# Optimization experiments

Measured on AMD Instinct MI355X. Metric: run time of the kernel, lower is better.

## Reference

```python
import jax, jax.numpy as jnp
import numpy as np

EMBED_DICT = 200
EMBED_DIM = 16
HIDDEN = 32
LSTM_DIM = 256
B, C, L = 8192, 16, 64
END_IDX = 1  # stand-in for token_list.index('<End>')


def _lin(k, i, o):
    return jax.random.normal(k, (i, o), jnp.float32) * (1.0 / np.sqrt(i))


def setup_inputs() -> dict:
    key = jax.random.key(0)
    ks = jax.random.split(key, 20)
    feat_in = EMBED_DIM * 14 + LSTM_DIM  # 480
    z = lambda n: jnp.zeros((n,), jnp.float32)
    return {
        "trees": jax.random.randint(ks[0], (B, 1 + C, 17), 0, L),
        "lstm_out_list": jax.random.normal(ks[1], (B, L, 1, LSTM_DIM), jnp.float32),
        "first_notes": jax.random.normal(ks[2], (B, EMBED_DIM), jnp.float32),
        "train": 1,
        "embedding": jax.random.normal(ks[3], (EMBED_DICT, EMBED_DIM), jnp.float32) * 0.05,
        "leaf_end_W": _lin(ks[4], EMBED_DIM, HIDDEN), "leaf_end_b": z(HIDDEN),
        "lc_W1": _lin(ks[5], feat_in, HIDDEN * 4), "lc_b1": z(HIDDEN * 4),
        "lc_W2": _lin(ks[6], HIDDEN * 4, HIDDEN), "lc_b2": z(HIDDEN),
        "cs_W1": _lin(ks[7], HIDDEN * 2, HIDDEN * 4), "cs_b1": z(HIDDEN * 4),
        "cs_W2": _lin(ks[8], HIDDEN * 4, HIDDEN), "cs_b2": z(HIDDEN),
        "nf_W1": _lin(ks[9], feat_in, HIDDEN * 4), "nf_b1": z(HIDDEN * 4),
        "nf_W2": _lin(ks[10], HIDDEN * 4, HIDDEN), "nf_b2": z(HIDDEN),
        "cb_W1": _lin(ks[11], HIDDEN * 2, HIDDEN * 4), "cb_b1": z(HIDDEN * 4),
        "cb_W2": _lin(ks[12], HIDDEN * 4, HIDDEN), "cb_b2": z(HIDDEN),
        "ff_W1": _lin(ks[13], HIDDEN, HIDDEN), "ff_b1": z(HIDDEN),
        "ff_W2": _lin(ks[14], HIDDEN, HIDDEN), "ff_b2": z(HIDDEN),
        "ts_W": _lin(ks[15], HIDDEN, 1), "ts_b": z(1),
    }


def _mlp2(x, W1, b1, W2, b2):
    # Linear -> ReLU -> Linear -> ReLU (matches nn.Sequential blocks)
    return jax.nn.relu(jax.nn.relu(x @ W1 + b1) @ W2 + b2)


def reference(trees, lstm_out_list, first_notes, train, embedding,
              leaf_end_W, leaf_end_b, lc_W1, lc_b1, lc_W2, lc_b2,
              cs_W1, cs_b1, cs_W2, cs_b2, nf_W1, nf_b1, nf_W2, nf_b2,
              cb_W1, cb_b1, cb_W2, cb_b2, ff_W1, ff_b1, ff_W2, ff_b2,
              ts_W, ts_b):
    Bn = trees.shape[0]
    root = trees[:, 0, :]        # (B, 17)
    leaves = trees[:, 1:, :]     # (B, C, 17)
    Cn = leaves.shape[1]
    bidx = jnp.arange(Bn)

    # ---- leaf nodes: either leaf_end_ff(embed(type)) or leaf_child_ff(concat) ----
    leaf_tok = embedding[leaves[:, :, 2:-1]].reshape(Bn, Cn, -1)       # (B,C,224)
    leaf_ptr = lstm_out_list[bidx[:, None], leaves[:, :, -1], 0, :]    # (B,C,256)
    leaf_child = _mlp2(jnp.concatenate([leaf_tok, leaf_ptr], -1),
                       lc_W1, lc_b1, lc_W2, lc_b2)                     # (B,C,32)
    leaf_end = embedding[leaves[:, :, 2]] @ leaf_end_W + leaf_end_b    # (B,C,32)
    is_end = (leaves[:, :, 2] == END_IDX)[..., None]
    children = jnp.where(is_end, leaf_end, leaf_child)                 # (B,C,32)

    # ---- sequential left fold with child_sum_ff over children ----
    def step(carry, child):
        nxt = _mlp2(jnp.concatenate([carry, child], -1), cs_W1, cs_b1, cs_W2, cs_b2)
        return nxt, None
    child_summary, _ = jax.lax.scan(step, children[:, 0],
                                    jnp.moveaxis(children[:, 1:], 0, 1))  # (B,32)

    # ---- root node embedding + combine ----
    node_tok = embedding[root[:, 2:-1]].reshape(Bn, -1)                # (B,224)
    node_ptr = lstm_out_list[bidx, root[:, -1], 0, :]                  # (B,256)
    node_tmp = _mlp2(jnp.concatenate([node_tok, node_ptr], -1),
                     nf_W1, nf_b1, nf_W2, nf_b2)                       # (B,32)
    tree_sum = _mlp2(jnp.concatenate([node_tmp, child_summary], -1),
                     cb_W1, cb_b1, cb_W2, cb_b2)                       # (B,32)

    # ---- head: two linears (no activation) then score ----
    ff = (tree_sum @ ff_W1 + ff_b1) @ ff_W2 + ff_b2
    return ff @ ts_W + ts_b                                            # (B,1)
```

## Files before the change

kernel.cpp:

```cpp
#include <hip/hip_runtime.h>
#include <cstddef>


typedef __bf16 bf16x8 __attribute__((ext_vector_type(8)));
typedef float  f32x4  __attribute__((ext_vector_type(4)));

__global__ __launch_bounds__(256) void prep_kernel(
    const float* __restrict__ embedding,
    const float* __restrict__ leaf_end_W, const float* __restrict__ leaf_end_b,
    const float* __restrict__ lc_W1, const float* __restrict__ lc_W2,
    const float* __restrict__ nf_W1, const float* __restrict__ nf_W2,
    const float* __restrict__ cs_W1, const float* __restrict__ cs_W2,
    const float* __restrict__ cb_W1, const float* __restrict__ cb_W2,
    const float* __restrict__ ff_W1, const float* __restrict__ ff_b1,
    const float* __restrict__ ff_W2, const float* __restrict__ ff_b2,
    const float* __restrict__ ts_W, const float* __restrict__ ts_b,
    __bf16* __restrict__ lcW1T, __bf16* __restrict__ nfW1T,
    __bf16* __restrict__ lcW2T, __bf16* __restrict__ nfW2T,
    __bf16* __restrict__ emb_bf, float* __restrict__ endvec,
    __bf16* __restrict__ csW1Th, __bf16* __restrict__ csW1Tl,
    __bf16* __restrict__ cbW1Th, __bf16* __restrict__ cbW1Tl,
    __bf16* __restrict__ csW2Th, __bf16* __restrict__ csW2Tl,
    __bf16* __restrict__ cbW2Th, __bf16* __restrict__ cbW2Tl,
    float* __restrict__ vfin, float* __restrict__ cfin)
{
    const int id = blockIdx.x * 256 + threadIdx.x;
    if (id < 61440) {
        const int n = id / 480, k = id - n * 480;
        lcW1T[id] = (__bf16)lc_W1[k * 128 + n];
    } else if (id < 122880) {
        const int e = id - 61440;
        const int n = e / 480, k = e - n * 480;
        nfW1T[e] = (__bf16)nf_W1[k * 128 + n];
    } else if (id < 126976) {
        const int e = id - 122880;
        const int n = e / 128, k = e - n * 128;
        lcW2T[e] = (__bf16)lc_W2[k * 32 + n];
    } else if (id < 131072) {
        const int e = id - 126976;
        const int n = e / 128, k = e - n * 128;
        nfW2T[e] = (__bf16)nf_W2[k * 32 + n];
    } else if (id < 134272) {
        emb_bf[id - 131072] = (__bf16)embedding[id - 131072];
    } else if (id < 134304) {
        const int c = id - 134272;
        float a = leaf_end_b[c];
        #pragma unroll
        for (int d = 0; d < 16; ++d) a = fmaf(embedding[16 + d], leaf_end_W[d * 32 + c], a);
        endvec[c] = a;
    } else if (id < 142496) {
        const int e = id - 134304;
        const int n = e >> 6, k = e & 63;
        const float v = cs_W1[k * 128 + n];
        const __bf16 h = (__bf16)v;
        csW1Th[e] = h; csW1Tl[e] = (__bf16)(v - (float)h);
    } else if (id < 150688) {
        const int e = id - 142496;
        const int n = e >> 6, k = e & 63;
        const float v = cb_W1[k * 128 + n];
        const __bf16 h = (__bf16)v;
        cbW1Th[e] = h; cbW1Tl[e] = (__bf16)(v - (float)h);
    } else if (id < 154784) {
        const int e = id - 150688;
        const int n = e >> 7, k = e & 127;
        const float v = cs_W2[k * 32 + n];
        const __bf16 h = (__bf16)v;
        csW2Th[e] = h; csW2Tl[e] = (__bf16)(v - (float)h);
    } else if (id < 158880) {
        const int e = id - 154784;
        const int n = e >> 7, k = e & 127;
        const float v = cb_W2[k * 32 + n];
        const __bf16 h = (__bf16)v;
        cbW2Th[e] = h; cbW2Tl[e] = (__bf16)(v - (float)h);
    } else if (id < 158912) {
        const int c = id - 158880;
        float w2t[32];
        #pragma unroll
        for (int k = 0; k < 32; ++k) {
            float a = 0.f;
            for (int j = 0; j < 32; ++j) a = fmaf(ff_W2[k * 32 + j], ts_W[j], a);
            w2t[k] = a;
        }
        float a = 0.f;
        #pragma unroll
        for (int k = 0; k < 32; ++k) a = fmaf(ff_W1[c * 32 + k], w2t[k], a);
        vfin[c] = a;
    } else if (id == 158912) {
        float a = ts_b[0];
        for (int j = 0; j < 32; ++j) a = fmaf(ff_b2[j], ts_W[j], a);
        for (int k = 0; k < 32; ++k) {
            float w2t = 0.f;
            for (int j = 0; j < 32; ++j) w2t = fmaf(ff_W2[k * 32 + j], ts_W[j], w2t);
            a = fmaf(ff_b1[k], w2t, a);
        }
        cfin[0] = a;
    }
}

__global__ __launch_bounds__(256) void mlp1_mfma(
    const int* __restrict__ trees,
    const float* __restrict__ lstm,
    const __bf16* __restrict__ lcW1T, const __bf16* __restrict__ nfW1T,
    const __bf16* __restrict__ lcW2T, const __bf16* __restrict__ nfW2T,
    const __bf16* __restrict__ emb_bf, const float* __restrict__ endvec,
    const float* __restrict__ lc_b1, const float* __restrict__ lc_b2,
    const float* __restrict__ nf_b1, const float* __restrict__ nf_b2,
    float* __restrict__ children,
    float* __restrict__ node_tmp)
{
    __shared__ __align__(16) __bf16 emb_s[3200];
    __shared__ __align__(16) __bf16 Hs[64][136];
    __shared__ float b1s[128], b2s[32], evs[32];
    __shared__ int   endf[64];

    const int tid = threadIdx.x;
    const int blk = blockIdx.x;
    const bool leaf = (blk < 2048);

    const __bf16* __restrict__ W1T = leaf ? lcW1T : nfW1T;
    const __bf16* __restrict__ W2T = leaf ? lcW2T : nfW2T;
    const float*  __restrict__ b1p = leaf ? lc_b1 : nf_b1;
    const float*  __restrict__ b2p = leaf ? lc_b2 : nf_b2;

    for (int i = tid; i < 3200; i += 256) emb_s[i] = emb_bf[i];
    if (tid < 128) b1s[tid] = b1p[tid];
    if (tid < 32)  { b2s[tid] = b2p[tid]; evs[tid] = leaf ? endvec[tid] : 0.f; }
    if (tid < 64) {
        if (leaf) {
            const int R = blk * 64 + tid;
            const int b = R >> 4, trow = 1 + (R & 15);
            endf[tid] = (trees[(b * 17 + trow) * 17 + 2] == 1);
        } else endf[tid] = 0;
    }

    const int l  = tid & 63;
    const int w  = tid >> 6;
    const int wm = w >> 1;
    const int wn = w & 1;
    const int lm = l & 15;
    const int kb = l >> 4;

    const int* tb[2];
    const float* lb[2];
    #pragma unroll
    for (int i = 0; i < 2; ++i) {
        const int r = wm * 32 + i * 16 + lm;
        int b, trow;
        if (leaf) { const int R = blk * 64 + r; b = R >> 4; trow = 1 + (R & 15); }
        else      { b = (blk - 2048) * 64 + r; trow = 0; }
        const int* t = trees + (b * 17 + trow) * 17;
        tb[i] = t;
        lb[i] = lstm + ((size_t)b * 64 + (size_t)t[16]) * 256;
    }

    f32x4 acc[2][4];
    #pragma unroll
    for (int i = 0; i < 2; ++i)
        #pragma unroll
        for (int j = 0; j < 4; ++j) acc[i][j] = (f32x4){0.f, 0.f, 0.f, 0.f};

    __syncthreads();

    #pragma unroll
    for (int c = 0; c < 15; ++c) {
        bf16x8 bfr[4];
        #pragma unroll
        for (int ct = 0; ct < 4; ++ct) {
            const int n = wn * 64 + ct * 16 + lm;
            bfr[ct] = *(const bf16x8*)(W1T + n * 480 + c * 32 + kb * 8);
        }
        bf16x8 afr[2];
        if (c < 7) {
            #pragma unroll
            for (int i = 0; i < 2; ++i) {
                const int tok = tb[i][2 + 2 * c + (kb >> 1)];
                afr[i] = *(const bf16x8*)(emb_s + tok * 16 + (kb & 1) * 8);
            }
        } else {
            #pragma unroll
            for (int i = 0; i < 2; ++i) {
                const float* p = lb[i] + (c - 7) * 32 + kb * 8;
                const float4 u = *(const float4*)p;
                const float4 v = *(const float4*)(p + 4);
                bf16x8 t;
                t[0] = (__bf16)u.x; t[1] = (__bf16)u.y; t[2] = (__bf16)u.z; t[3] = (__bf16)u.w;
                t[4] = (__bf16)v.x; t[5] = (__bf16)v.y; t[6] = (__bf16)v.z; t[7] = (__bf16)v.w;
                afr[i] = t;
            }
        }
        #pragma unroll
        for (int i = 0; i < 2; ++i)
            #pragma unroll
            for (int ct = 0; ct < 4; ++ct)
                acc[i][ct] = __builtin_amdgcn_mfma_f32_16x16x32_bf16(afr[i], bfr[ct], acc[i][ct], 0, 0, 0);
    }

    #pragma unroll
    for (int i = 0; i < 2; ++i)
        #pragma unroll
        for (int ct = 0; ct < 4; ++ct) {
            const int col = wn * 64 + ct * 16 + lm;
            const float bias = b1s[col];
            #pragma unroll
            for (int rg = 0; rg < 4; ++rg) {
                float v = acc[i][ct][rg] + bias;
                v = v > 0.f ? v : 0.f;
                Hs[wm * 32 + i * 16 + 4 * kb + rg][col] = (__bf16)v;
            }
        }
    __syncthreads();

    f32x4 acc2[2];
    acc2[0] = (f32x4){0.f, 0.f, 0.f, 0.f};
    acc2[1] = (f32x4){0.f, 0.f, 0.f, 0.f};

    #pragma unroll
    for (int kc = 0; kc < 4; ++kc) {
        const bf16x8 a2 = *(const bf16x8*)(&Hs[w * 16 + lm][kc * 32 + kb * 8]);
        #pragma unroll
        for (int j = 0; j < 2; ++j) {
            const bf16x8 b2 = *(const bf16x8*)(W2T + (j * 16 + lm) * 128 + kc * 32 + kb * 8);
            acc2[j] = __builtin_amdgcn_mfma_f32_16x16x32_bf16(a2, b2, acc2[j], 0, 0, 0);
        }
    }

    #pragma unroll
    for (int j = 0; j < 2; ++j) {
        const int col = j * 16 + lm;
        const float bias = b2s[col];
        #pragma unroll
        for (int rg = 0; rg < 4; ++rg) {
            const int row = w * 16 + 4 * kb + rg;
            float v = acc2[j][rg] + bias;
            v = v > 0.f ? v : 0.f;
            if (leaf) {
                const size_t R = (size_t)blk * 64 + row;
                children[R * 32 + col] = endf[row] ? evs[col] : v;
            } else {
                const size_t R = (size_t)(blk - 2048) * 64 + row;
                node_tmp[R * 32 + col] = v;
            }
        }
    }
}

__global__ __launch_bounds__(512) void scan_mfma(
    const float* __restrict__ children,
    const float* __restrict__ node_tmp,
    const __bf16* __restrict__ csW1Th, const __bf16* __restrict__ csW1Tl,
    const __bf16* __restrict__ csW2Th, const __bf16* __restrict__ csW2Tl,
    const __bf16* __restrict__ cbW1Th, const __bf16* __restrict__ cbW1Tl,
    const __bf16* __restrict__ cbW2Th, const __bf16* __restrict__ cbW2Tl,
    const float* __restrict__ cs_b1, const float* __restrict__ cs_b2,
    const float* __restrict__ cb_b1, const float* __restrict__ cb_b2,
    const float* __restrict__ vfin_g, const float* __restrict__ cfin_g,
    float* __restrict__ out)
{
    __shared__ __align__(16) __bf16 Xh[64][72], Xl[64][72];
    __shared__ __align__(16) __bf16 Hh[64][136], Hl[64][136];
    __shared__ float b1a[128], b1b[128], b2a[32], b2b[32], vfin[32];
    __shared__ float psum[2][64];
    __shared__ float cfin_s;

    const int tid = threadIdx.x;
    const int l = tid & 63, w = tid >> 6;
    const int lm = l & 15, kb = l >> 4;

    if (tid < 128)      { b1a[tid] = cs_b1[tid]; b1b[tid] = cb_b1[tid]; }
    else if (tid < 160) { b2a[tid - 128] = cs_b2[tid - 128]; b2b[tid - 128] = cb_b2[tid - 128]; }
    else if (tid < 192) { vfin[tid - 160] = vfin_g[tid - 160]; }
    else if (tid == 192) cfin_s = cfin_g[0];

    bf16x8 W1r[2][2][2];
    {
        const int q = w & 3;
        #pragma unroll
        for (int nt = 0; nt < 2; ++nt)
            #pragma unroll
            for (int kc = 0; kc < 2; ++kc) {
                const int n = q * 32 + nt * 16 + lm;
                W1r[nt][kc][0] = *(const bf16x8*)(csW1Th + n * 64 + kc * 32 + kb * 8);
                W1r[nt][kc][1] = *(const bf16x8*)(csW1Tl + n * 64 + kc * 32 + kb * 8);
            }
    }
    bf16x8 W2r[4][2];
    {
        const int n2 = (w & 1) * 16 + lm;
        #pragma unroll
        for (int kc = 0; kc < 4; ++kc) {
            W2r[kc][0] = *(const bf16x8*)(csW2Th + n2 * 128 + kc * 32 + kb * 8);
            W2r[kc][1] = *(const bf16x8*)(csW2Tl + n2 * 128 + kc * 32 + kb * 8);
        }
    }

    const size_t base = (size_t)blockIdx.x * 64;
    const int tt = tid >> 3, c4 = (tid & 7) * 4;

    {
        const float4 v0 = *(const float4*)&children[((base + tt) * 16 + 0) * 32 + c4];
        const float4 v1 = *(const float4*)&children[((base + tt) * 16 + 1) * 32 + c4];
        const float a0[4] = {v0.x, v0.y, v0.z, v0.w};
        const float a1[4] = {v1.x, v1.y, v1.z, v1.w};
        union { __bf16 b[4]; short4 s; } h0, l0, h1, l1;
        #pragma unroll
        for (int j = 0; j < 4; ++j) {
            h0.b[j] = (__bf16)a0[j]; l0.b[j] = (__bf16)(a0[j] - (float)h0.b[j]);
            h1.b[j] = (__bf16)a1[j]; l1.b[j] = (__bf16)(a1[j] - (float)h1.b[j]);
        }
        *(short4*)&Xh[tt][c4]      = h0.s;
        *(short4*)&Xl[tt][c4]      = l0.s;
        *(short4*)&Xh[tt][32 + c4] = h1.s;
        *(short4*)&Xl[tt][32 + c4] = l1.s;
    }
    __syncthreads();

    #pragma unroll 1
    for (int it = 1; it <= 16; ++it) {
        const bool fin = (it == 16);
        if (fin) {
            const int q = w & 3;
            #pragma unroll
            for (int nt = 0; nt < 2; ++nt)
                #pragma unroll
                for (int kc = 0; kc < 2; ++kc) {
                    const int n = q * 32 + nt * 16 + lm;
                    W1r[nt][kc][0] = *(const bf16x8*)(cbW1Th + n * 64 + kc * 32 + kb * 8);
                    W1r[nt][kc][1] = *(const bf16x8*)(cbW1Tl + n * 64 + kc * 32 + kb * 8);
                }
            const int n2 = (w & 1) * 16 + lm;
            #pragma unroll
            for (int kc = 0; kc < 4; ++kc) {
                W2r[kc][0] = *(const bf16x8*)(cbW2Th + n2 * 128 + kc * 32 + kb * 8);
                W2r[kc][1] = *(const bf16x8*)(cbW2Tl + n2 * 128 + kc * 32 + kb * 8);
            }
        }
        const float* __restrict__ b1c = fin ? b1b : b1a;
        const float* __restrict__ b2c = fin ? b2b : b2a;

        float4 pf;
        const int pfmode = (it < 15) ? 1 : (it == 15 ? 2 : 0);
        if (pfmode == 1)      pf = *(const float4*)&children[((base + tt) * 16 + (it + 1)) * 32 + c4];
        else if (pfmode == 2) pf = *(const float4*)&node_tmp[(base + tt) * 32 + c4];

        const int mh = w >> 2, q = w & 3;
        bf16x8 xh[2][2], xl[2][2];
        #pragma unroll
        for (int i = 0; i < 2; ++i)
            #pragma unroll
            for (int kc = 0; kc < 2; ++kc) {
                const int row = mh * 32 + i * 16 + lm;
                xh[i][kc] = *(const bf16x8*)&Xh[row][kc * 32 + kb * 8];
                xl[i][kc] = *(const bf16x8*)&Xl[row][kc * 32 + kb * 8];
            }
        f32x4 a1[2][2];
        #pragma unroll
        for (int i = 0; i < 2; ++i)
            #pragma unroll
            for (int nt = 0; nt < 2; ++nt) {
                a1[i][nt] = (f32x4){0.f, 0.f, 0.f, 0.f};
                #pragma unroll
                for (int kc = 0; kc < 2; ++kc) {
                    a1[i][nt] = __builtin_amdgcn_mfma_f32_16x16x32_bf16(xh[i][kc], W1r[nt][kc][0], a1[i][nt], 0, 0, 0);
                    a1[i][nt] = __builtin_amdgcn_mfma_f32_16x16x32_bf16(xl[i][kc], W1r[nt][kc][0], a1[i][nt], 0, 0, 0);
                    a1[i][nt] = __builtin_amdgcn_mfma_f32_16x16x32_bf16(xh[i][kc], W1r[nt][kc][1], a1[i][nt], 0, 0, 0);
                }
            }
        #pragma unroll
        for (int i = 0; i < 2; ++i)
            #pragma unroll
            for (int nt = 0; nt < 2; ++nt) {
                const int col = q * 32 + nt * 16 + lm;
                const float bias = b1c[col];
                #pragma unroll
                for (int rg = 0; rg < 4; ++rg) {
                    const int row = mh * 32 + i * 16 + 4 * kb + rg;
                    float v = a1[i][nt][rg] + bias;
                    v = v > 0.f ? v : 0.f;
                    const __bf16 h = (__bf16)v;
                    Hh[row][col] = h;
                    Hl[row][col] = (__bf16)(v - (float)h);
                }
            }
        __syncthreads();

        const int mt = w >> 1;
        f32x4 a2 = (f32x4){0.f, 0.f, 0.f, 0.f};
        #pragma unroll
        for (int kc = 0; kc < 4; ++kc) {
            const bf16x8 ah = *(const bf16x8*)&Hh[mt * 16 + lm][kc * 32 + kb * 8];
            const bf16x8 al = *(const bf16x8*)&Hl[mt * 16 + lm][kc * 32 + kb * 8];
            a2 = __builtin_amdgcn_mfma_f32_16x16x32_bf16(ah, W2r[kc][0], a2, 0, 0, 0);
            a2 = __builtin_amdgcn_mfma_f32_16x16x32_bf16(al, W2r[kc][0], a2, 0, 0, 0);
            a2 = __builtin_amdgcn_mfma_f32_16x16x32_bf16(ah, W2r[kc][1], a2, 0, 0, 0);
        }

        if (!fin) {
            const int cb_ = (it == 15) ? 32 : 0;
            const int col = (w & 1) * 16 + lm;
            const float bias = b2c[col];
            #pragma unroll
            for (int rg = 0; rg < 4; ++rg) {
                const int row = mt * 16 + 4 * kb + rg;
                float v = a2[rg] + bias;
                v = v > 0.f ? v : 0.f;
                const __bf16 h = (__bf16)v;
                Xh[row][cb_ + col] = h;
                Xl[row][cb_ + col] = (__bf16)(v - (float)h);
            }
            if (pfmode) {
                const int dst = (pfmode == 2) ? 0 : 32;
                const float a0[4] = {pf.x, pf.y, pf.z, pf.w};
                union { __bf16 b[4]; short4 s; } hh, ll;
                #pragma unroll
                for (int j = 0; j < 4; ++j) {
                    hh.b[j] = (__bf16)a0[j]; ll.b[j] = (__bf16)(a0[j] - (float)hh.b[j]);
                }
                *(short4*)&Xh[tt][dst + c4] = hh.s;
                *(short4*)&Xl[tt][dst + c4] = ll.s;
            }
            __syncthreads();
        } else {
            const int col = (w & 1) * 16 + lm;
            const float bias = b2c[col];
            const float vf = vfin[col];
            float part[4];
            #pragma unroll
            for (int rg = 0; rg < 4; ++rg) {
                float v = a2[rg] + bias;
                v = v > 0.f ? v : 0.f;
                part[rg] = v * vf;
            }
            #pragma unroll
            for (int m = 1; m < 16; m <<= 1)
                #pragma unroll
                for (int rg = 0; rg < 4; ++rg)
                    part[rg] += __shfl_xor(part[rg], m, 64);
            if (lm == 0) {
                #pragma unroll
                for (int rg = 0; rg < 4; ++rg)
                    psum[w & 1][mt * 16 + 4 * kb + rg] = part[rg];
            }
            __syncthreads();
            if (tid < 64) out[base + tid] = cfin_s + psum[0][tid] + psum[1][tid];
        }
    }
}

extern "C" void kernel_launch(void* const* d_in, const int* in_sizes, int n_in,
                              void* d_out, int out_size, void* d_ws, size_t ws_size,
                              hipStream_t stream) {
    const int*   trees      = (const int*)d_in[0];
    const float* lstm       = (const float*)d_in[1];
    const float* embedding  = (const float*)d_in[4];
    const float* leaf_end_W = (const float*)d_in[5];
    const float* leaf_end_b = (const float*)d_in[6];
    const float* lc_W1 = (const float*)d_in[7];
    const float* lc_b1 = (const float*)d_in[8];
    const float* lc_W2 = (const float*)d_in[9];
    const float* lc_b2 = (const float*)d_in[10];
    const float* cs_W1 = (const float*)d_in[11];
    const float* cs_b1 = (const float*)d_in[12];
    const float* cs_W2 = (const float*)d_in[13];
    const float* cs_b2 = (const float*)d_in[14];
    const float* nf_W1 = (const float*)d_in[15];
    const float* nf_b1 = (const float*)d_in[16];
    const float* nf_W2 = (const float*)d_in[17];
    const float* nf_b2 = (const float*)d_in[18];
    const float* cb_W1 = (const float*)d_in[19];
    const float* cb_b1 = (const float*)d_in[20];
    const float* cb_W2 = (const float*)d_in[21];
    const float* cb_b2 = (const float*)d_in[22];
    const float* ff_W1 = (const float*)d_in[23];
    const float* ff_b1 = (const float*)d_in[24];
    const float* ff_W2 = (const float*)d_in[25];
    const float* ff_b2 = (const float*)d_in[26];
    const float* ts_W  = (const float*)d_in[27];
    const float* ts_b  = (const float*)d_in[28];

    char* ws = (char*)d_ws;
    float*  children = (float*)ws;
    float*  node_tmp = (float*)(ws + 16777216);
    __bf16* lcW1T    = (__bf16*)(ws + 17825792);
    __bf16* nfW1T    = (__bf16*)(ws + 17948672);
    __bf16* lcW2T    = (__bf16*)(ws + 18071552);
    __bf16* nfW2T    = (__bf16*)(ws + 18079744);
    __bf16* emb_bf   = (__bf16*)(ws + 18087936);
    float*  endvec   = (float*)(ws + 18094336);
    __bf16* csW1Th   = (__bf16*)(ws + 18094464);
    __bf16* csW1Tl   = (__bf16*)(ws + 18110848);
    __bf16* cbW1Th   = (__bf16*)(ws + 18127232);
    __bf16* cbW1Tl   = (__bf16*)(ws + 18143616);
    __bf16* csW2Th   = (__bf16*)(ws + 18160000);
    __bf16* csW2Tl   = (__bf16*)(ws + 18168192);
    __bf16* cbW2Th   = (__bf16*)(ws + 18176384);
    __bf16* cbW2Tl   = (__bf16*)(ws + 18184576);
    float*  vfin     = (float*)(ws + 18192768);
    float*  cfin     = (float*)(ws + 18192896);
    float*  outp     = (float*)d_out;

    prep_kernel<<<dim3(621), dim3(256), 0, stream>>>(
        embedding, leaf_end_W, leaf_end_b, lc_W1, lc_W2, nf_W1, nf_W2,
        cs_W1, cs_W2, cb_W1, cb_W2, ff_W1, ff_b1, ff_W2, ff_b2, ts_W, ts_b,
        lcW1T, nfW1T, lcW2T, nfW2T, emb_bf, endvec,
        csW1Th, csW1Tl, cbW1Th, cbW1Tl, csW2Th, csW2Tl, cbW2Th, cbW2Tl,
        vfin, cfin);

    mlp1_mfma<<<dim3(2176), dim3(256), 0, stream>>>(
        trees, lstm, lcW1T, nfW1T, lcW2T, nfW2T, emb_bf, endvec,
        lc_b1, lc_b2, nf_b1, nf_b2, children, node_tmp);

    scan_mfma<<<dim3(128), dim3(512), 0, stream>>>(
        children, node_tmp,
        csW1Th, csW1Tl, csW2Th, csW2Tl, cbW1Th, cbW1Tl, cbW2Th, cbW2Tl,
        cs_b1, cs_b2, cb_b1, cb_b2, vfin, cfin, outp);
}
```

Before: 136.4 us.

## Store intermediates as split bf16 pairs and halve scan block size

The first MLP kernel now writes children and node_tmp as high/low bf16 pairs instead of fp32, moving the split conversion out of the serial scan kernel. The scan kernel processes 32 rows per block with 256 threads across 256 blocks instead of 64 rows with 512 threads across 128 blocks, which spreads the latency-bound sequential fold over more CUs. The mlp1 kernel also gets a min-blocks-per-CU launch bound of 4. Total intermediate bytes stay the same, but the split now happens at write time.

```diff
diff --git a/kernel.cpp b/kernel.cpp
--- a/kernel.cpp
+++ b/kernel.cpp
@@ -3,6 +3,7 @@
 
 
 typedef __bf16 bf16x8 __attribute__((ext_vector_type(8)));
+typedef __bf16 bf16x4 __attribute__((ext_vector_type(4)));
 typedef float  f32x4  __attribute__((ext_vector_type(4)));
 
 __global__ __launch_bounds__(256) void prep_kernel(
@@ -97,7 +98,7 @@
     }
 }
 
-__global__ __launch_bounds__(256) void mlp1_mfma(
+__global__ __launch_bounds__(256, 4) void mlp1_mfma(
     const int* __restrict__ trees,
     const float* __restrict__ lstm,
     const __bf16* __restrict__ lcW1T, const __bf16* __restrict__ nfW1T,
@@ -105,8 +106,8 @@
     const __bf16* __restrict__ emb_bf, const float* __restrict__ endvec,
     const float* __restrict__ lc_b1, const float* __restrict__ lc_b2,
     const float* __restrict__ nf_b1, const float* __restrict__ nf_b2,
-    float* __restrict__ children,
-    float* __restrict__ node_tmp)
+    __bf16* __restrict__ childrenH, __bf16* __restrict__ childrenL,
+    __bf16* __restrict__ node_tmpH, __bf16* __restrict__ node_tmpL)
 {
     __shared__ __align__(16) __bf16 emb_s[3200];
     __shared__ __align__(16) __bf16 Hs[64][136];
@@ -233,20 +234,25 @@
             const int row = w * 16 + 4 * kb + rg;
             float v = acc2[j][rg] + bias;
             v = v > 0.f ? v : 0.f;
+            if (leaf && endf[row]) v = evs[col];
+            const __bf16 h  = (__bf16)v;
+            const __bf16 lo = (__bf16)(v - (float)h);
             if (leaf) {
                 const size_t R = (size_t)blk * 64 + row;
-                children[R * 32 + col] = endf[row] ? evs[col] : v;
+                childrenH[R * 32 + col] = h;
+                childrenL[R * 32 + col] = lo;
             } else {
                 const size_t R = (size_t)(blk - 2048) * 64 + row;
-                node_tmp[R * 32 + col] = v;
+                node_tmpH[R * 32 + col] = h;
+                node_tmpL[R * 32 + col] = lo;
             }
         }
     }
 }
 
-__global__ __launch_bounds__(512) void scan_mfma(
-    const float* __restrict__ children,
-    const float* __restrict__ node_tmp,
+__global__ __launch_bounds__(256) void scan_mfma(
+    const __bf16* __restrict__ childrenH, const __bf16* __restrict__ childrenL,
+    const __bf16* __restrict__ node_tmpH, const __bf16* __restrict__ node_tmpL,
     const __bf16* __restrict__ csW1Th, const __bf16* __restrict__ csW1Tl,
     const __bf16* __restrict__ csW2Th, const __bf16* __restrict__ csW2Tl,
     const __bf16* __restrict__ cbW1Th, const __bf16* __restrict__ cbW1Tl,
@@ -256,10 +262,10 @@
     const float* __restrict__ vfin_g, const float* __restrict__ cfin_g,
     float* __restrict__ out)
 {
-    __shared__ __align__(16) __bf16 Xh[64][72], Xl[64][72];
-    __shared__ __align__(16) __bf16 Hh[64][136], Hl[64][136];
+    __shared__ __align__(16) __bf16 Xh[32][72], Xl[32][72];
+    __shared__ __align__(16) __bf16 Hh[32][136], Hl[32][136];
     __shared__ float b1a[128], b1b[128], b2a[32], b2b[32], vfin[32];
-    __shared__ float psum[2][64];
+    __shared__ float psum[2][32];
     __shared__ float cfin_s;
 
     const int tid = threadIdx.x;
@@ -273,12 +279,11 @@
 
     bf16x8 W1r[2][2][2];
     {
-        const int q = w & 3;
         #pragma unroll
         for (int nt = 0; nt < 2; ++nt)
             #pragma unroll
             for (int kc = 0; kc < 2; ++kc) {
-                const int n = q * 32 + nt * 16 + lm;
+                const int n = w * 32 + nt * 16 + lm;
                 W1r[nt][kc][0] = *(const bf16x8*)(csW1Th + n * 64 + kc * 32 + kb * 8);
                 W1r[nt][kc][1] = *(const bf16x8*)(csW1Tl + n * 64 + kc * 32 + kb * 8);
             }
@@ -293,24 +298,16 @@
         }
     }
 
-    const size_t base = (size_t)blockIdx.x * 64;
+    const size_t base = (size_t)blockIdx.x * 32;
     const int tt = tid >> 3, c4 = (tid & 7) * 4;
 
     {
-        const float4 v0 = *(const float4*)&children[((base + tt) * 16 + 0) * 32 + c4];
-        const float4 v1 = *(const float4*)&children[((base + tt) * 16 + 1) * 32 + c4];
-        const float a0[4] = {v0.x, v0.y, v0.z, v0.w};
-        const float a1[4] = {v1.x, v1.y, v1.z, v1.w};
-        union { __bf16 b[4]; short4 s; } h0, l0, h1, l1;
-        #pragma unroll
-        for (int j = 0; j < 4; ++j) {
-            h0.b[j] = (__bf16)a0[j]; l0.b[j] = (__bf16)(a0[j] - (float)h0.b[j]);
-            h1.b[j] = (__bf16)a1[j]; l1.b[j] = (__bf16)(a1[j] - (float)h1.b[j]);
-        }
-        *(short4*)&Xh[tt][c4]      = h0.s;
-        *(short4*)&Xl[tt][c4]      = l0.s;
-        *(short4*)&Xh[tt][32 + c4] = h1.s;
-        *(short4*)&Xl[tt][32 + c4] = l1.s;
+        const size_t o0 = ((base + tt) * 16 + 0) * 32 + c4;
+        const size_t o1 = ((base + tt) * 16 + 1) * 32 + c4;
+        *(bf16x4*)&Xh[tt][c4]      = *(const bf16x4*)(childrenH + o0);
+        *(bf16x4*)&Xl[tt][c4]      = *(const bf16x4*)(childrenL + o0);
+        *(bf16x4*)&Xh[tt][32 + c4] = *(const bf16x4*)(childrenH + o1);
+        *(bf16x4*)&Xl[tt][32 + c4] = *(const bf16x4*)(childrenL + o1);
     }
     __syncthreads();
 
@@ -318,12 +315,11 @@
     for (int it = 1; it <= 16; ++it) {
         const bool fin = (it == 16);
         if (fin) {
-            const int q = w & 3;
             #pragma unroll
             for (int nt = 0; nt < 2; ++nt)
                 #pragma unroll
                 for (int kc = 0; kc < 2; ++kc) {
-                    const int n = q * 32 + nt * 16 + lm;
+                    const int n = w * 32 + nt * 16 + lm;
                     W1r[nt][kc][0] = *(const bf16x8*)(cbW1Th + n * 64 + kc * 32 + kb * 8);
                     W1r[nt][kc][1] = *(const bf16x8*)(cbW1Tl + n * 64 + kc * 32 + kb * 8);
                 }
@@ -337,18 +333,24 @@
         const float* __restrict__ b1c = fin ? b1b : b1a;
         const float* __restrict__ b2c = fin ? b2b : b2a;
 
-        float4 pf;
+        bf16x4 pfh, pfl;
         const int pfmode = (it < 15) ? 1 : (it == 15 ? 2 : 0);
-        if (pfmode == 1)      pf = *(const float4*)&children[((base + tt) * 16 + (it + 1)) * 32 + c4];
-        else if (pfmode == 2) pf = *(const float4*)&node_tmp[(base + tt) * 32 + c4];
-
-        const int mh = w >> 2, q = w & 3;
+        if (pfmode == 1) {
+            const size_t o = ((base + tt) * 16 + (it + 1)) * 32 + c4;
+            pfh = *(const bf16x4*)(childrenH + o);
+            pfl = *(const bf16x4*)(childrenL + o);
+        } else if (pfmode == 2) {
+            const size_t o = (base + tt) * 32 + c4;
+            pfh = *(const bf16x4*)(node_tmpH + o);
+            pfl = *(const bf16x4*)(node_tmpL + o);
+        }
+
         bf16x8 xh[2][2], xl[2][2];
         #pragma unroll
         for (int i = 0; i < 2; ++i)
             #pragma unroll
             for (int kc = 0; kc < 2; ++kc) {
-                const int row = mh * 32 + i * 16 + lm;
+                const int row = i * 16 + lm;
                 xh[i][kc] = *(const bf16x8*)&Xh[row][kc * 32 + kb * 8];
                 xl[i][kc] = *(const bf16x8*)&Xl[row][kc * 32 + kb * 8];
             }
@@ -369,11 +371,11 @@
         for (int i = 0; i < 2; ++i)
             #pragma unroll
             for (int nt = 0; nt < 2; ++nt) {
-                const int col = q * 32 + nt * 16 + lm;
+                const int col = w * 32 + nt * 16 + lm;
                 const float bias = b1c[col];
                 #pragma unroll
                 for (int rg = 0; rg < 4; ++rg) {
-                    const int row = mh * 32 + i * 16 + 4 * kb + rg;
+                    const int row = i * 16 + 4 * kb + rg;
                     float v = a1[i][nt][rg] + bias;
                     v = v > 0.f ? v : 0.f;
                     const __bf16 h = (__bf16)v;
@@ -409,14 +411,8 @@
             }
             if (pfmode) {
                 const int dst = (pfmode == 2) ? 0 : 32;
-                const float a0[4] = {pf.x, pf.y, pf.z, pf.w};
-                union { __bf16 b[4]; short4 s; } hh, ll;
-                #pragma unroll
-                for (int j = 0; j < 4; ++j) {
-                    hh.b[j] = (__bf16)a0[j]; ll.b[j] = (__bf16)(a0[j] - (float)hh.b[j]);
-                }
-                *(short4*)&Xh[tt][dst + c4] = hh.s;
-                *(short4*)&Xl[tt][dst + c4] = ll.s;
+                *(bf16x4*)&Xh[tt][dst + c4] = pfh;
+                *(bf16x4*)&Xl[tt][dst + c4] = pfl;
             }
             __syncthreads();
         } else {
@@ -441,7 +437,7 @@
                     psum[w & 1][mt * 16 + 4 * kb + rg] = part[rg];
             }
             __syncthreads();
-            if (tid < 64) out[base + tid] = cfin_s + psum[0][tid] + psum[1][tid];
+            if (tid < 32) out[base + tid] = cfin_s + psum[0][tid] + psum[1][tid];
         }
     }
 }
@@ -478,8 +474,10 @@
     const float* ts_b  = (const float*)d_in[28];
 
     char* ws = (char*)d_ws;
-    float*  children = (float*)ws;
-    float*  node_tmp = (float*)(ws + 16777216);
+    __bf16* childrenH = (__bf16*)ws;
+    __bf16* childrenL = (__bf16*)(ws + 8388608);
+    __bf16* node_tmpH = (__bf16*)(ws + 16777216);
+    __bf16* node_tmpL = (__bf16*)(ws + 17301504);
     __bf16* lcW1T    = (__bf16*)(ws + 17825792);
     __bf16* nfW1T    = (__bf16*)(ws + 17948672);
     __bf16* lcW2T    = (__bf16*)(ws + 18071552);
@@ -507,10 +505,10 @@
 
     mlp1_mfma<<<dim3(2176), dim3(256), 0, stream>>>(
         trees, lstm, lcW1T, nfW1T, lcW2T, nfW2T, emb_bf, endvec,
-        lc_b1, lc_b2, nf_b1, nf_b2, children, node_tmp);
-
-    scan_mfma<<<dim3(128), dim3(512), 0, stream>>>(
-        children, node_tmp,
+        lc_b1, lc_b2, nf_b1, nf_b2, childrenH, childrenL, node_tmpH, node_tmpL);
+
+    scan_mfma<<<dim3(256), dim3(256), 0, stream>>>(
+        childrenH, childrenL, node_tmpH, node_tmpL,
         csW1Th, csW1Tl, csW2Th, csW2Tl, cbW1Th, cbW1Tl, cbW2Th, cbW2Tl,
         cs_b1, cs_b2, cb_b1, cb_b2, vfin, cfin, outp);
 }
```

Measured after the change: 129.3 us. -5.2%, faster.
